# Optimization experiments

Hardware: AMD Instinct MI355X
Metric: run time of the kernel (lower is better)

## Reference

```python
import jax, jax.numpy as jnp
import numpy as np

B = 131072
D = 256  # embedding_dim
P = 64   # prosody / accent feature dim

# per-speaker prosody constants from the hardcoded 4-speaker table
PITCH_TAB = jnp.array([120.0, 100.0, 220.0, 190.0], dtype=jnp.float32) / 200.0
ENERGY_TAB = jnp.array([0.8, 0.6, 0.85, 0.7], dtype=jnp.float32)
RATE_TAB = jnp.array([1.1, 0.9, 1.15, 1.0], dtype=jnp.float32)


def setup_inputs() -> dict:
    key = jax.random.key(0)
    ks = jax.random.split(key, 16)
    s = 0.05
    return {
        "speaker_id": jax.random.randint(ks[0], (B,), 0, 4, dtype=jnp.int64),
        "emotion_embedding": jax.random.normal(ks[1], (B, D), dtype=jnp.float32),
        "accent_level": 1,
        "emb_table": jax.random.normal(ks[2], (4, D), dtype=jnp.float32),
        "pitch_w": jax.random.normal(ks[3], (P,), dtype=jnp.float32) * s,
        "pitch_b": jax.random.normal(ks[4], (P,), dtype=jnp.float32) * s,
        "energy_w": jax.random.normal(ks[5], (P,), dtype=jnp.float32) * s,
        "energy_b": jax.random.normal(ks[6], (P,), dtype=jnp.float32) * s,
        "rate_w": jax.random.normal(ks[7], (P,), dtype=jnp.float32) * s,
        "rate_b": jax.random.normal(ks[8], (P,), dtype=jnp.float32) * s,
        "accent_table": jax.random.normal(ks[9], (3, P), dtype=jnp.float32),
        "w1": jax.random.normal(ks[10], (D + 3 * P + P, D), dtype=jnp.float32) * s,
        "b1": jnp.zeros((D,), dtype=jnp.float32),
        "ln_g": jnp.ones((D,), dtype=jnp.float32),
        "ln_b": jnp.zeros((D,), dtype=jnp.float32),
        "w2": jax.random.normal(ks[11], (D, D), dtype=jnp.float32) * s,
        "b2": jnp.zeros((D,), dtype=jnp.float32),
        "emo_w": jax.random.normal(ks[12], (D, D), dtype=jnp.float32) * s,
        "emo_b": jnp.zeros((D,), dtype=jnp.float32),
    }


def reference(speaker_id, emotion_embedding, accent_level, emb_table,
              pitch_w, pitch_b, energy_w, energy_b, rate_w, rate_b,
              accent_table, w1, b1, ln_g, ln_b, w2, b2, emo_w, emo_b):
    b = speaker_id.shape[0]
    speaker_embed = emb_table[speaker_id]  # [B, D]
    # vectorized replacement of the per-sample prosody loop: Linear(1,64) == outer product
    pitch_feat = PITCH_TAB[speaker_id][:, None] * pitch_w[None, :] + pitch_b
    energy_feat = ENERGY_TAB[speaker_id][:, None] * energy_w[None, :] + energy_b
    rate_feat = RATE_TAB[speaker_id][:, None] * rate_w[None, :] + rate_b
    prosody = jnp.concatenate([pitch_feat, energy_feat, rate_feat], axis=1)  # [B, 192]
    accent_embed = jnp.broadcast_to(accent_table[accent_level][None, :], (b, P))
    combined = jnp.concatenate([speaker_embed, prosody, accent_embed], axis=1)  # [B, 512]
    h = jax.nn.relu(combined @ w1 + b1)
    # LayerNorm (eps=1e-5)
    mu = jnp.mean(h, axis=-1, keepdims=True)
    var = jnp.mean(jnp.square(h - mu), axis=-1, keepdims=True)
    h = (h - mu) * jax.lax.rsqrt(var + 1e-5) * ln_g + ln_b
    out = h @ w2 + b2
    out = out + 0.3 * (emotion_embedding @ emo_w + emo_b)
    # F.normalize(dim=-1)
    norm = jnp.maximum(jnp.linalg.norm(out, axis=-1, keepdims=True), 1e-12)
    return out / norm
```

## Files before the change

kernel.cpp:

```cpp
#include <hip/hip_runtime.h>
#include <hip/hip_bf16.h>

typedef __attribute__((ext_vector_type(8))) short bf16x8;
typedef __attribute__((ext_vector_type(4))) float f32x4;
typedef const __attribute__((address_space(1))) unsigned int* gas_u32p;
typedef __attribute__((address_space(3))) unsigned int* las_u32p;

static __device__ inline short f2bf(float f) {
    __hip_bfloat16 h = __float2bfloat16(f);
    return *reinterpret_cast<short*>(&h);
}

__global__ __launch_bounds__(1024) void setup_kernel(
    const float* __restrict__ emb_table,
    const float* __restrict__ pitch_w, const float* __restrict__ pitch_b,
    const float* __restrict__ energy_w, const float* __restrict__ energy_b,
    const float* __restrict__ rate_w, const float* __restrict__ rate_b,
    const float* __restrict__ accent_table, const int* __restrict__ accent_level,
    const float* __restrict__ w1, const float* __restrict__ b1,
    const float* __restrict__ ln_g, const float* __restrict__ ln_b,
    const float* __restrict__ w2, const float* __restrict__ b2,
    const float* __restrict__ emo_w, const float* __restrict__ emo_b,
    float* __restrict__ base_out, unsigned short* __restrict__ wpack)
{
    if (blockIdx.x < 4) {
        const int s = blockIdx.x;
        __shared__ float comb[512];
        __shared__ float part[4][256];
        __shared__ float redS[16];
        __shared__ float redQ[16];
        __shared__ float hbuf[256];
        const int t = threadIdx.x;
        const int n = t & 255;
        const int kp = t >> 8;

        if (t < 512) {
            const int i = t;
            float v;
            if (i < 256) {
                v = emb_table[s * 256 + i];
            } else if (i < 320) {
                float pt = (s == 0) ? 0.6f : (s == 1) ? 0.5f : (s == 2) ? 1.1f : 0.95f;
                v = pt * pitch_w[i - 256] + pitch_b[i - 256];
            } else if (i < 384) {
                float et = (s == 0) ? 0.8f : (s == 1) ? 0.6f : (s == 2) ? 0.85f : 0.7f;
                v = et * energy_w[i - 320] + energy_b[i - 320];
            } else if (i < 448) {
                float rt = (s == 0) ? 1.1f : (s == 1) ? 0.9f : (s == 2) ? 1.15f : 1.0f;
                v = rt * rate_w[i - 384] + rate_b[i - 384];
            } else {
                v = accent_table[accent_level[0] * 64 + (i - 448)];
            }
            comb[i] = v;
        }
        __syncthreads();

        float hp = 0.f;
        {
            const int k0 = kp * 128;
            #pragma unroll 8
            for (int k = 0; k < 128; ++k)
                hp = fmaf(comb[k0 + k], w1[(size_t)(k0 + k) * 256 + n], hp);
        }
        part[kp][n] = hp;
        __syncthreads();

        float h = b1[n] + part[0][n] + part[1][n] + part[2][n] + part[3][n];
        h = fmaxf(h, 0.f);

        float sum = h, sq = h * h;
        for (int m = 32; m; m >>= 1) {
            sum += __shfl_xor(sum, m, 64);
            sq  += __shfl_xor(sq, m, 64);
        }
        if ((t & 63) == 0) { redS[t >> 6] = sum; redQ[t >> 6] = sq; }
        __syncthreads();
        const float tot = redS[0] + redS[1] + redS[2] + redS[3];
        const float tsq = redQ[0] + redQ[1] + redQ[2] + redQ[3];
        const float mu  = tot * (1.0f / 256.0f);
        const float var = tsq * (1.0f / 256.0f) - mu * mu;
        const float hn = (h - mu) * rsqrtf(var + 1e-5f) * ln_g[n] + ln_b[n];
        if (t < 256) hbuf[n] = hn;
        __syncthreads();

        float op = 0.f;
        {
            const int k0 = kp * 64;
            #pragma unroll 8
            for (int k = 0; k < 64; ++k)
                op = fmaf(hbuf[k0 + k], w2[(size_t)(k0 + k) * 256 + n], op);
        }
        part[kp][n] = op;
        __syncthreads();
        if (t < 256) {
            base_out[s * 256 + n] = b2[n] + 0.3f * emo_b[n]
                                  + part[0][n] + part[1][n] + part[2][n] + part[3][n];
        }
    } else {
        const int idx = (blockIdx.x - 4) * 1024 + threadIdx.x;
        const int l  = idx & 63;
        const int ks = (idx >> 6) & 7;
        const int ct = idx >> 9;
        const int col = ct * 16 + (l & 15);
        const int kb  = ks * 32 + (l >> 4) * 8;
        bf16x8 pk;
        #pragma unroll
        for (int j = 0; j < 8; ++j) pk[j] = f2bf(emo_w[(size_t)(kb + j) * 256 + col]);
        *reinterpret_cast<bf16x8*>(wpack + (size_t)idx * 8) = pk;
    }
}

__global__ __launch_bounds__(1024, 4) void main_kernel(
    const float* __restrict__ emo, const int* __restrict__ sid,
    const float* __restrict__ base, const unsigned short* __restrict__ wpack,
    float* __restrict__ out)
{
    extern __shared__ unsigned short sB[];
    const int tid = threadIdx.x;
    const int wave = tid >> 6;
    const int lane = tid & 63;
    const int arow = lane & 15;
    const int agrp = lane >> 4;
    const unsigned short* bptr = sB + lane * 8;

    #pragma unroll
    for (int p = 0; p < 8; ++p) {
        const int e = p * 1024 + tid;
        __builtin_amdgcn_global_load_lds((gas_u32p)wpack + e * 4,
                                         (las_u32p)sB + e * 4, 16, 0, 0);
    }

    auto load_convert = [&](int row0, bf16x8* af) {
        const float* aptr = emo + (size_t)(row0 + arow) * 256 + agrp * 8;
        f32x4 t0[8], t1[8];
        #pragma unroll
        for (int ks = 0; ks < 8; ++ks) {
            t0[ks] = *reinterpret_cast<const f32x4*>(aptr + ks * 32);
            t1[ks] = *reinterpret_cast<const f32x4*>(aptr + ks * 32 + 4);
        }
        #pragma unroll
        for (int ks = 0; ks < 8; ++ks) {
            af[ks][0] = f2bf(t0[ks][0]); af[ks][1] = f2bf(t0[ks][1]);
            af[ks][2] = f2bf(t0[ks][2]); af[ks][3] = f2bf(t0[ks][3]);
            af[ks][4] = f2bf(t1[ks][0]); af[ks][5] = f2bf(t1[ks][1]);
            af[ks][6] = f2bf(t1[ks][2]); af[ks][7] = f2bf(t1[ks][3]);
        }
    };

    auto run_mfma = [&](const bf16x8* af, f32x4* acc) {
        #pragma unroll
        for (int ks = 0; ks < 8; ++ks) {
            #pragma unroll
            for (int ct = 0; ct < 16; ++ct) {
                bf16x8 bfr = *reinterpret_cast<const bf16x8*>(bptr + ((ct * 8 + ks) << 9));
                acc[ct] = __builtin_amdgcn_mfma_f32_16x16x32_bf16(af[ks], bfr, acc[ct], 0, 0, 0);
            }
        }
    };

    auto epilogue = [&](int row0, f32x4* acc) {
        int sidv[4];
        #pragma unroll
        for (int j = 0; j < 4; ++j) sidv[j] = sid[row0 + agrp * 4 + j];
        float p[4] = {0.f, 0.f, 0.f, 0.f};
        #pragma unroll
        for (int ct = 0; ct < 16; ++ct) {
            #pragma unroll
            for (int j = 0; j < 4; ++j) {
                float pre = fmaf(0.3f, acc[ct][j], base[sidv[j] * 256 + ct * 16 + arow]);
                acc[ct][j] = pre;
                p[j] = fmaf(pre, pre, p[j]);
            }
        }
        #pragma unroll
        for (int j = 0; j < 4; ++j) {
            p[j] += __shfl_xor(p[j], 1, 64);
            p[j] += __shfl_xor(p[j], 2, 64);
            p[j] += __shfl_xor(p[j], 4, 64);
            p[j] += __shfl_xor(p[j], 8, 64);
            p[j] = 1.0f / fmaxf(sqrtf(p[j]), 1e-12f);
        }
        #pragma unroll
        for (int ct = 0; ct < 16; ++ct) {
            #pragma unroll
            for (int j = 0; j < 4; ++j) {
                out[(size_t)(row0 + agrp * 4 + j) * 256 + ct * 16 + arow] = acc[ct][j] * p[j];
            }
        }
    };

    const int rowbase = blockIdx.x * 512 + wave * 16;
    const f32x4 zero = {0.f, 0.f, 0.f, 0.f};

    bf16x8 af0[8];
    load_convert(rowbase, af0);
    __syncthreads();

    f32x4 acc[16];
    #pragma unroll
    for (int i = 0; i < 16; ++i) acc[i] = zero;
    run_mfma(af0, acc);
    epilogue(rowbase, acc);

    bf16x8 af1[8];
    load_convert(rowbase + 256, af1);
    #pragma unroll
    for (int i = 0; i < 16; ++i) acc[i] = zero;
    run_mfma(af1, acc);
    epilogue(rowbase + 256, acc);
}

extern "C" void kernel_launch(void* const* d_in, const int* in_sizes, int n_in,
                              void* d_out, int out_size, void* d_ws, size_t ws_size,
                              hipStream_t stream) {
    const int*   sid          = (const int*)d_in[0];
    const float* emo          = (const float*)d_in[1];
    const int*   accent_level = (const int*)d_in[2];
    const float* emb_table    = (const float*)d_in[3];
    const float* pitch_w      = (const float*)d_in[4];
    const float* pitch_b      = (const float*)d_in[5];
    const float* energy_w     = (const float*)d_in[6];
    const float* energy_b     = (const float*)d_in[7];
    const float* rate_w       = (const float*)d_in[8];
    const float* rate_b       = (const float*)d_in[9];
    const float* accent_table = (const float*)d_in[10];
    const float* w1           = (const float*)d_in[11];
    const float* b1           = (const float*)d_in[12];
    const float* ln_g         = (const float*)d_in[13];
    const float* ln_b         = (const float*)d_in[14];
    const float* w2           = (const float*)d_in[15];
    const float* b2           = (const float*)d_in[16];
    const float* emo_w        = (const float*)d_in[17];
    const float* emo_b        = (const float*)d_in[18];

    float* base = (float*)d_ws;
    unsigned short* wpack = (unsigned short*)((char*)d_ws + 4096);

    const int B = in_sizes[0];

    setup_kernel<<<12, 1024, 0, stream>>>(emb_table, pitch_w, pitch_b, energy_w, energy_b,
                                          rate_w, rate_b, accent_table, accent_level,
                                          w1, b1, ln_g, ln_b, w2, b2, emo_w, emo_b,
                                          base, wpack);
    main_kernel<<<B / 512, 1024, 131072, stream>>>(emo, sid, base, wpack, (float*)d_out);
}
```

Baseline: 310.8 us.

## Halve block size and software-pipeline emotion row loads across four passes

```diff
diff --git a/kernel.cpp b/kernel.cpp
--- a/kernel.cpp
+++ b/kernel.cpp
@@ -110,7 +110,7 @@
     }
 }
 
-__global__ __launch_bounds__(1024, 4) void main_kernel(
+__global__ __launch_bounds__(512, 2) void main_kernel(
     const float* __restrict__ emo, const int* __restrict__ sid,
     const float* __restrict__ base, const unsigned short* __restrict__ wpack,
     float* __restrict__ out)
@@ -124,26 +124,32 @@
     const unsigned short* bptr = sB + lane * 8;
 
     #pragma unroll
-    for (int p = 0; p < 8; ++p) {
-        const int e = p * 1024 + tid;
+    for (int p = 0; p < 16; ++p) {
+        const int e = p * 512 + tid;
         __builtin_amdgcn_global_load_lds((gas_u32p)wpack + e * 4,
                                          (las_u32p)sB + e * 4, 16, 0, 0);
     }
 
-    auto load_convert = [&](int row0, bf16x8* af) {
+    auto row_of = [&](int pass) {
+        return blockIdx.x * 512 + pass * 128 + wave * 16;
+    };
+
+    auto load_raw = [&](int row0, f32x4* t) {
         const float* aptr = emo + (size_t)(row0 + arow) * 256 + agrp * 8;
-        f32x4 t0[8], t1[8];
         #pragma unroll
         for (int ks = 0; ks < 8; ++ks) {
-            t0[ks] = *reinterpret_cast<const f32x4*>(aptr + ks * 32);
-            t1[ks] = *reinterpret_cast<const f32x4*>(aptr + ks * 32 + 4);
-        }
+            t[2 * ks]     = *reinterpret_cast<const f32x4*>(aptr + ks * 32);
+            t[2 * ks + 1] = *reinterpret_cast<const f32x4*>(aptr + ks * 32 + 4);
+        }
+    };
+
+    auto cvt = [&](const f32x4* t, bf16x8* af) {
         #pragma unroll
         for (int ks = 0; ks < 8; ++ks) {
-            af[ks][0] = f2bf(t0[ks][0]); af[ks][1] = f2bf(t0[ks][1]);
-            af[ks][2] = f2bf(t0[ks][2]); af[ks][3] = f2bf(t0[ks][3]);
-            af[ks][4] = f2bf(t1[ks][0]); af[ks][5] = f2bf(t1[ks][1]);
-            af[ks][6] = f2bf(t1[ks][2]); af[ks][7] = f2bf(t1[ks][3]);
+            af[ks][0] = f2bf(t[2*ks][0]);   af[ks][1] = f2bf(t[2*ks][1]);
+            af[ks][2] = f2bf(t[2*ks][2]);   af[ks][3] = f2bf(t[2*ks][3]);
+            af[ks][4] = f2bf(t[2*ks+1][0]); af[ks][5] = f2bf(t[2*ks+1][1]);
+            af[ks][6] = f2bf(t[2*ks+1][2]); af[ks][7] = f2bf(t[2*ks+1][3]);
         }
     };
 
@@ -189,25 +195,40 @@
         }
     };
 
-    const int rowbase = blockIdx.x * 512 + wave * 16;
     const f32x4 zero = {0.f, 0.f, 0.f, 0.f};
-
-    bf16x8 af0[8];
-    load_convert(rowbase, af0);
+    f32x4 tA[16], tB[16];
+    bf16x8 af[8];
+    f32x4 acc[16];
+
+    load_raw(row_of(0), tA);
     __syncthreads();
 
-    f32x4 acc[16];
-    #pragma unroll
-    for (int i = 0; i < 16; ++i) acc[i] = zero;
-    run_mfma(af0, acc);
-    epilogue(rowbase, acc);
-
-    bf16x8 af1[8];
-    load_convert(rowbase + 256, af1);
-    #pragma unroll
-    for (int i = 0; i < 16; ++i) acc[i] = zero;
-    run_mfma(af1, acc);
-    epilogue(rowbase + 256, acc);
+    cvt(tA, af);
+    load_raw(row_of(1), tB);
+    #pragma unroll
+    for (int i = 0; i < 16; ++i) acc[i] = zero;
+    run_mfma(af, acc);
+    epilogue(row_of(0), acc);
+
+    cvt(tB, af);
+    load_raw(row_of(2), tA);
+    #pragma unroll
+    for (int i = 0; i < 16; ++i) acc[i] = zero;
+    run_mfma(af, acc);
+    epilogue(row_of(1), acc);
+
+    cvt(tA, af);
+    load_raw(row_of(3), tB);
+    #pragma unroll
+    for (int i = 0; i < 16; ++i) acc[i] = zero;
+    run_mfma(af, acc);
+    epilogue(row_of(2), acc);
+
+    cvt(tB, af);
+    #pragma unroll
+    for (int i = 0; i < 16; ++i) acc[i] = zero;
+    run_mfma(af, acc);
+    epilogue(row_of(3), acc);
 }
 
 extern "C" void kernel_launch(void* const* d_in, const int* in_sizes, int n_in,
@@ -242,5 +263,5 @@
                                           rate_w, rate_b, accent_table, accent_level,
                                           w1, b1, ln_g, ln_b, w2, b2, emo_w, emo_b,
                                           base, wpack);
-    main_kernel<<<B / 512, 1024, 131072, stream>>>(emo, sid, base, wpack, (float*)d_out);
-}
+    main_kernel<<<B / 512, 512, 131072, stream>>>(emo, sid, base, wpack, (float*)d_out);
+}
```

After: 310.8 us. About the same (+0.0%).
